# Performance work log

Hardware: AMD Instinct MI355X
Metric: run time of the kernel (lower is better)

The kernel has to match this reference:

```python
import jax, jax.numpy as jnp
import numpy as np

CLIP_LEN = 16
IN_CH = 64  # math.ceil(256 // 4 / 4) * 4
BN_EPS = 1e-5


def setup_inputs() -> dict:
    key = jax.random.key(0)
    ks = jax.random.split(key, 7)
    x = jax.random.normal(ks[0], (128, 256, 56, 56), jnp.float32)
    bn_gamma = 1.0 + 0.1 * jax.random.normal(ks[1], (IN_CH,), jnp.float32)
    bn_beta = 0.1 * jax.random.normal(ks[2], (IN_CH,), jnp.float32)
    bn_mean = 0.1 * jax.random.normal(ks[3], (IN_CH,), jnp.float32)
    bn_var = jax.random.uniform(ks[4], (IN_CH,), jnp.float32, minval=0.5, maxval=1.5)
    # groups=2 Conv3d: out=2, in_per_group=IN_CH//2, kernel 3x3x3
    conv_w = 0.02 * jax.random.normal(ks[5], (2, IN_CH // 2, 3, 3, 3), jnp.float32)
    conv_b = 0.02 * jax.random.normal(ks[6], (2,), jnp.float32)
    return dict(x=x, bn_gamma=bn_gamma, bn_beta=bn_beta, bn_mean=bn_mean,
                bn_var=bn_var, conv_w=conv_w, conv_b=conv_b)


def _gsm(x5, bn_gamma, bn_beta, bn_mean, bn_var, conv_w, conv_b):
    # x5: [n, c, t, h, w] with c == IN_CH
    n, c, t, h, w = x5.shape
    scale = bn_gamma * jax.lax.rsqrt(bn_var + BN_EPS)          # [c]
    shift = bn_beta - bn_mean * scale                          # [c]
    x_act = jax.nn.relu(x5 * scale[None, :, None, None, None]
                        + shift[None, :, None, None, None])
    gate = jnp.tanh(
        jax.lax.conv_general_dilated(
            x_act, conv_w, window_strides=(1, 1, 1), padding='SAME',
            dimension_numbers=('NCDHW', 'OIDHW', 'NCDHW'),
            feature_group_count=2)
        + conv_b[None, :, None, None, None])                   # [n,2,t,h,w]
    half = c // 2

    def gated_shift(xg, g, left):
        y = g * xg                                             # gated part
        r = xg - y                                             # residual part
        if left:
            y_sh = jnp.concatenate([y[:, :, 1:], jnp.zeros_like(y[:, :, :1])], axis=2)
        else:
            y_sh = jnp.concatenate([jnp.zeros_like(y[:, :, :1]), y[:, :, :-1]], axis=2)
        out = y_sh + r
        # channel regroup: [n,2,c/4,t,h,w] -> permute -> [n,c/2,t,h,w]
        return out.reshape(n, 2, half // 2, t, h, w).transpose(0, 2, 1, 3, 4, 5).reshape(n, half, t, h, w)

    y1 = gated_shift(x5[:, :half], gate[:, 0:1], left=True)
    y2 = gated_shift(x5[:, half:], gate[:, 1:2], left=False)
    return jnp.concatenate([y1, y2], axis=1)


def reference(x, bn_gamma, bn_beta, bn_mean, bn_var, conv_w, conv_b):
    nt, c, h, w = x.shape
    n = nt // CLIP_LEN
    # [nt, IN_CH, h, w] -> [n, IN_CH, T, h, w]
    xs = x[:, :IN_CH].reshape(n, CLIP_LEN, IN_CH, h, w).transpose(0, 2, 1, 3, 4)
    y = _gsm(xs, bn_gamma, bn_beta, bn_mean, bn_var, conv_w, conv_b)
    y = y.transpose(0, 2, 1, 3, 4).reshape(nt, IN_CH, h, w)
    # remaining channels pass through unchanged; net wrapper is identity
    return jnp.concatenate([y, x[:, IN_CH:]], axis=1)
```

## Files before the change

### kernel.cpp

```cpp
#include <hip/hip_runtime.h>
#include <math.h>

namespace {
constexpr int kT = 16;
constexpr int kH = 56;
constexpr int kW = 56;
constexpr int kCAll = 256;
constexpr int kPlane = kH * kW;
constexpr int kPlane4 = kPlane / 4;
constexpr size_t kGateBytes = (size_t)256 * kPlane * sizeof(float);
constexpr int kSpan = 192 * kPlane4;
constexpr int kFrame4 = kCAll * kPlane4;

typedef float nt4 __attribute__((ext_vector_type(4)));
}

__device__ __forceinline__ float4 nt_load4(const float4* p) {
  nt4 v = __builtin_nontemporal_load(reinterpret_cast<const nt4*>(p));
  return make_float4(v.x, v.y, v.z, v.w);
}
__device__ __forceinline__ void nt_store4(const float4& a, float4* p) {
  nt4 v = {a.x, a.y, a.z, a.w};
  __builtin_nontemporal_store(v, reinterpret_cast<nt4*>(p));
}


__device__ __forceinline__ void conv_block(
    int bid, int tid, const float* __restrict__ x,
    const float* __restrict__ gamma, const float* __restrict__ beta,
    const float* __restrict__ mean, const float* __restrict__ var,
    const float* __restrict__ cw, const float* __restrict__ cb,
    float* __restrict__ gate, float4* smb) {
  const int stripe = bid & 1;
  const int g = (bid >> 1) & 1;
  const int t = (bid >> 2) & 15;
  const int n = bid >> 6;
  const int h0 = stripe * 28;
  const int wid = tid >> 6;
  const int lane = tid & 63;
  const int r = lane >> 1;
  const int h = lane & 1;
  const int wbase = wid * 510;

  for (int i = lane; i < 510; i += 64)
    smb[wbase + i] = make_float4(0.f, 0.f, 0.f, 0.f);

  int rr_u[7], fb_u[7], go_u[7];
  bool val_u[7];
  #pragma unroll
  for (int u = 0; u < 7; ++u) {
    const int j = lane + u * 64;
    bool v = (j < 420);
    int rr = 0, fb = 0, go = 0;
    if (v) {
      rr = j / 14;
      fb = j - rr * 14;
      const int gr = h0 + rr - 1;
      v = ((unsigned)gr < (unsigned)kH);
      if (v) go = gr * 14 + fb;
    }
    rr_u[u] = rr; fb_u[u] = fb; go_u[u] = go; val_u[u] = v;
  }

  float acc[28];
  #pragma unroll
  for (int p = 0; p < 28; ++p) acc[p] = 0.f;

  auto loadS = [&](int s, float4 (&pf)[7]) {
    const int il = s / 3;
    const int kd = s - il * 3;
    const int tt = t + kd - 1;
    const int ch = g * 32 + wid * 8 + il;
    if (tt >= 0 && tt < kT) {
      const float4* src4 =
          (const float4*)x + ((size_t)(n * kT + tt) * kCAll + ch) * kPlane4;
      #pragma unroll
      for (int u = 0; u < 7; ++u)
        pf[u] = val_u[u] ? src4[go_u[u]] : make_float4(0.f, 0.f, 0.f, 0.f);
    } else {
      #pragma unroll
      for (int u = 0; u < 7; ++u) pf[u] = make_float4(0.f, 0.f, 0.f, 0.f);
    }
  };

  auto stageS = [&](int s, const float4 (&pf)[7]) {
    const int il = s / 3;
    const int kd = s - il * 3;
    const int tt = t + kd - 1;
    if (tt < 0 || tt >= kT) return;
    const int ch = g * 32 + wid * 8 + il;
    const float sc = gamma[ch] * rsqrtf(var[ch] + 1e-5f);
    const float sh = beta[ch] - mean[ch] * sc;
    #pragma unroll
    for (int u = 0; u < 7; ++u) {
      if (val_u[u]) {
        float4 a = pf[u];
        a.x = fmaxf(0.f, fmaf(a.x, sc, sh));
        a.y = fmaxf(0.f, fmaf(a.y, sc, sh));
        a.z = fmaxf(0.f, fmaf(a.z, sc, sh));
        a.w = fmaxf(0.f, fmaf(a.w, sc, sh));
        smb[wbase + rr_u[u] * 17 + fb_u[u] + 1] = a;
      }
    }
  };

  auto computeS = [&](int s) {
    const int il = s / 3;
    const int kd = s - il * 3;
    const int tt = t + kd - 1;
    if (tt < 0 || tt >= kT) return;
    if (r >= 28) return;
    const int ch = g * 32 + wid * 8 + il;
    const float* wbp = cw + ch * 27 + kd * 9;
    float wk[9];
    #pragma unroll
    for (int j = 0; j < 9; ++j) wk[j] = wbp[j];
    #pragma unroll
    for (int kh = 0; kh < 3; ++kh) {
      const int base = wbase + (r + kh) * 17 + 7 * h;
      float f[36];
      #pragma unroll
      for (int jj = 0; jj < 9; ++jj) {
        const float4 B = smb[base + jj];
        f[4 * jj + 0] = B.x; f[4 * jj + 1] = B.y;
        f[4 * jj + 2] = B.z; f[4 * jj + 3] = B.w;
      }
      const float w0 = wk[kh * 3 + 0];
      const float w1 = wk[kh * 3 + 1];
      const float w2 = wk[kh * 3 + 2];
      #pragma unroll
      for (int p = 0; p < 28; ++p)
        acc[p] = fmaf(f[p + 3], w0,
                 fmaf(f[p + 4], w1, fmaf(f[p + 5], w2, acc[p])));
    }
  };

  float4 A[7], B[7];
  loadS(0, A);
  for (int s2 = 0; s2 < 24; s2 += 2) {
    if (s2 + 1 < 24) loadS(s2 + 1, B);
    stageS(s2, A);
    computeS(s2);
    if (s2 + 2 < 24) loadS(s2 + 2, A);
    if (s2 + 1 < 24) { stageS(s2 + 1, B); computeS(s2 + 1); }
  }

  __syncthreads();
  float* smf = (float*)smb;
  if (r < 28) {
    const int q0 = r * 56 + h * 28;
    #pragma unroll
    for (int p = 0; p < 28; ++p) smf[wid * 1568 + q0 + p] = acc[p];
  }
  __syncthreads();
  const float bias = cb[g];
  float* gp = gate + ((size_t)(n * 2 + g) * kT + t) * kPlane + h0 * kW;
  for (int q = tid; q < 1568; q += 256) {
    float s = smf[q] + smf[1568 + q] + smf[2 * 1568 + q] + smf[3 * 1568 + q];
    gp[q] = tanhf(s + bias);
  }
}

__device__ __forceinline__ void copy_engine(
    int engine, int nengines, int tid, const float4* __restrict__ x4,
    float4* __restrict__ o4, int nf, int skip_hole) {
  const int wave = engine * 4 + (tid >> 6);
  const int lane = tid & 63;
  const int nwaves = nengines * 4;
  const size_t nsb = (size_t)nf * (kSpan / 512);
  for (size_t sb = wave; sb < nsb; sb += nwaves) {
    const size_t base = sb * 512 + lane;
    const int f = (int)(base / kSpan);
    const int within = (int)(base - (size_t)f * kSpan);
    const size_t gbase = (size_t)f * kFrame4 + 64 * kPlane4 + within;
    float4 v[8];
    #pragma unroll
    for (int u = 0; u < 8; ++u) v[u] = nt_load4(&x4[gbase + u * 64]);
    if (!skip_hole || f != 126) {
      #pragma unroll
      for (int u = 0; u < 8; ++u) nt_store4(v[u], &o4[gbase + u * 64]);
    } else {
      #pragma unroll
      for (int u = 0; u < 8; ++u)
        if (within + u * 64 >= 3 * kPlane4) nt_store4(v[u], &o4[gbase + u * 64]);
    }
  }
}

__global__ __launch_bounds__(256, 2)
void fused_conv_copy_kernel(const float* __restrict__ x,
                            const float* __restrict__ gamma,
                            const float* __restrict__ beta,
                            const float* __restrict__ mean,
                            const float* __restrict__ var,
                            const float* __restrict__ cw,
                            const float* __restrict__ cb,
                            float* __restrict__ gate,
                            const float4* __restrict__ x4,
                            float4* __restrict__ o4,
                            int nf_copy, int skip_hole) {
  __shared__ float4 smb[4 * 510];
  if ((blockIdx.x & 1) == 0) {
    copy_engine(blockIdx.x >> 1, 512, threadIdx.x, x4, o4, nf_copy, skip_hole);
    return;
  }
  conv_block(blockIdx.x >> 1, threadIdx.x, x, gamma, beta, mean, var, cw, cb,
             gate, smb);
}

__global__ __launch_bounds__(256)
void shift_columns_kernel(const float4* __restrict__ x4,
                          const float4* __restrict__ g4,
                          float4* __restrict__ o4) {
  const int q = blockIdx.x * 256 + threadIdx.x;
  const size_t xstep = (size_t)kFrame4;
  const int p = q % kPlane4;
  const int rem = q / kPlane4;
  const int m = rem & 31;
  const int half = (rem >> 5) & 1;
  const int n = rem >> 6;
  const int src_ch = half * 32 + m;
  const int k = 2 * (m & 15) + (m >> 4);
  const int c = half * 32 + k;
  const float4* xp = x4 + ((size_t)(n * kT) * kCAll + src_ch) * kPlane4 + p;
  const float4* gp = g4 + (size_t)((n * 2 + half) * kT) * kPlane4 + p;
  float4* op = o4 + ((size_t)(n * kT) * kCAll + c) * kPlane4 + p;
  if (half == 0) {
    float4 xc = nt_load4(&xp[0]);
    float4 gc = gp[0];
    #pragma unroll
    for (int t = 0; t < kT; ++t) {
      float4 xn = make_float4(0.f, 0.f, 0.f, 0.f);
      float4 gn = make_float4(0.f, 0.f, 0.f, 0.f);
      if (t < kT - 1) {
        xn = nt_load4(&xp[(size_t)(t + 1) * xstep]);
        gn = gp[(t + 1) * kPlane4];
      }
      float4 res;
      res.x = gn.x * xn.x + xc.x - gc.x * xc.x;
      res.y = gn.y * xn.y + xc.y - gc.y * xc.y;
      res.z = gn.z * xn.z + xc.z - gc.z * xc.z;
      res.w = gn.w * xn.w + xc.w - gc.w * xc.w;
      nt_store4(res, &op[(size_t)t * xstep]);
      xc = xn; gc = gn;
    }
  } else {
    float4 xprev = make_float4(0.f, 0.f, 0.f, 0.f);
    float4 gprev = make_float4(0.f, 0.f, 0.f, 0.f);
    #pragma unroll
    for (int t = 0; t < kT; ++t) {
      const float4 xc = nt_load4(&xp[(size_t)t * xstep]);
      const float4 gc = gp[t * kPlane4];
      float4 res;
      res.x = gprev.x * xprev.x + xc.x - gc.x * xc.x;
      res.y = gprev.y * xprev.y + xc.y - gc.y * xc.y;
      res.z = gprev.z * xprev.z + xc.z - gc.z * xc.z;
      res.w = gprev.w * xprev.w + xc.w - gc.w * xc.w;
      nt_store4(res, &op[(size_t)t * xstep]);
      xprev = xc; gprev = gc;
    }
  }
}

__global__ __launch_bounds__(256)
void copy_gate_slice_kernel(float4* __restrict__ o4) {
  const int j = blockIdx.x * 256 + threadIdx.x;
  if (j >= 3 * kPlane4) return;
  const int q = j / kPlane4;
  const int rr = j - q * kPlane4;
  const int pidx = (q == 0) ? 239 : (q == 1 ? 254 : 255);
  const size_t G1 = (size_t)127 * kCAll * kPlane4;
  const size_t H = ((size_t)126 * kCAll + 64) * kPlane4;
  o4[H + j] = o4[G1 + (size_t)pidx * kPlane4 + rr];
}

__global__ __launch_bounds__(256)
void shift_c64_kernel(const float4* __restrict__ x4,
                      const float4* __restrict__ g4,
                      float4* __restrict__ o4, int nf) {
  const size_t total = (size_t)nf * 64 * kPlane4;
  const size_t j = (size_t)blockIdx.x * 256 + threadIdx.x;
  if (j >= total) return;
  const int p = (int)(j % kPlane4);
  const size_t rest = j / kPlane4;
  const int c = (int)(rest % 64);
  const int f = (int)(rest / 64);
  const int n = f >> 4;
  const int t = f & 15;
  const int half = c >> 5;
  const int k = c & 31;
  const int m = ((k & 1) << 4) + (k >> 1);
  const int src_ch = half * 32 + m;
  const size_t xcur = ((size_t)f * kCAll + src_ch) * kPlane4 + p;
  const size_t gbase = (size_t)(n * 2 + half) * kT * kPlane4 + p;
  const float4 xc = x4[xcur];
  const float4 gc = g4[gbase + (size_t)t * kPlane4];
  float4 y = make_float4(0.f, 0.f, 0.f, 0.f);
  if (half == 0) {
    if (t < kT - 1) {
      const float4 xn = x4[xcur + (size_t)kCAll * kPlane4];
      const float4 gn = g4[gbase + (size_t)(t + 1) * kPlane4];
      y.x = gn.x * xn.x; y.y = gn.y * xn.y; y.z = gn.z * xn.z; y.w = gn.w * xn.w;
    }
  } else {
    if (t > 0) {
      const float4 xp = x4[xcur - (size_t)kCAll * kPlane4];
      const float4 gp = g4[gbase + (size_t)(t - 1) * kPlane4];
      y.x = gp.x * xp.x; y.y = gp.y * xp.y; y.z = gp.z * xp.z; y.w = gp.w * xp.w;
    }
  }
  const size_t oidx = ((size_t)f * kCAll + c) * kPlane4 + p;
  float4 res;
  res.x = y.x + (xc.x - gc.x * xc.x);
  res.y = y.y + (xc.y - gc.y * xc.y);
  res.z = y.z + (xc.z - gc.z * xc.z);
  res.w = y.w + (xc.w - gc.w * xc.w);
  o4[oidx] = res;
}

__global__ __launch_bounds__(256)
void last_frame_kernel(const float4* __restrict__ x4, float4* o4) {
  const int idx = blockIdx.x * 256 + threadIdx.x;
  if (idx >= kCAll * kPlane4) return;
  const size_t F127 = (size_t)127 * kCAll * kPlane4;
  const int p = idx % kPlane4;
  const int c = idx / kPlane4;
  if (c >= 64) { o4[F127 + idx] = x4[F127 + idx]; return; }
  const size_t H = ((size_t)126 * kCAll + 64) * kPlane4;
  const int half = c >> 5;
  const int k = c & 31;
  const int m = ((k & 1) << 4) + (k >> 1);
  const int src_ch = half * 32 + m;
  const float4 xc = x4[F127 + (size_t)src_ch * kPlane4 + p];
  float4 gc;
  float4 y = make_float4(0.f, 0.f, 0.f, 0.f);
  if (half == 0) {
    gc = o4[H + 0 * kPlane4 + p];
  } else {
    gc = o4[H + 2 * kPlane4 + p];
    const float4 gp = o4[H + 1 * kPlane4 + p];
    const float4 xp = x4[((size_t)126 * kCAll + src_ch) * kPlane4 + p];
    y.x = gp.x * xp.x; y.y = gp.y * xp.y; y.z = gp.z * xp.z; y.w = gp.w * xp.w;
  }
  float4 res;
  res.x = y.x + (xc.x - gc.x * xc.x);
  res.y = y.y + (xc.y - gc.y * xc.y);
  res.z = y.z + (xc.z - gc.z * xc.z);
  res.w = y.w + (xc.w - gc.w * xc.w);
  o4[F127 + idx] = res;
}

__global__ __launch_bounds__(256)
void fix_hole_kernel(const float4* __restrict__ x4, float4* __restrict__ o4) {
  const int j = blockIdx.x * 256 + threadIdx.x;
  if (j >= 3 * kPlane4) return;
  const size_t H = ((size_t)126 * kCAll + 64) * kPlane4;
  o4[H + j] = x4[H + j];
}

extern "C" void kernel_launch(void* const* d_in, const int* in_sizes, int n_in,
                              void* d_out, int out_size, void* d_ws, size_t ws_size,
                              hipStream_t stream) {
  const float* x     = (const float*)d_in[0];
  const float* gamma = (const float*)d_in[1];
  const float* beta  = (const float*)d_in[2];
  const float* mean  = (const float*)d_in[3];
  const float* var   = (const float*)d_in[4];
  const float* cw    = (const float*)d_in[5];
  const float* cb    = (const float*)d_in[6];
  float* out = (float*)d_out;
  const float4* x4v = (const float4*)x;
  float4* o4v = (float4*)out;

  const bool have_ws = (d_ws != nullptr) && (ws_size >= kGateBytes);
  float* gate = have_ws ? (float*)d_ws : out + (size_t)127 * kCAll * kPlane;
  const int nf = have_ws ? 128 : 127;
  const int skip_hole = have_ws ? 0 : 1;

  fused_conv_copy_kernel<<<1024, 256, 0, stream>>>(
      x, gamma, beta, mean, var, cw, cb, gate, x4v, o4v, nf, skip_hole);

  if (have_ws) {
    shift_columns_kernel<<<1568, 256, 0, stream>>>(
        x4v, (const float4*)gate, o4v);
  } else {
    copy_gate_slice_kernel<<<10, 256, 0, stream>>>(o4v);
    const int shift_total = nf * 64 * kPlane4;
    shift_c64_kernel<<<(shift_total + 255) / 256, 256, 0, stream>>>(
        x4v, (const float4*)gate, o4v, nf);
    last_frame_kernel<<<(kCAll * kPlane4 + 255) / 256, 256, 0, stream>>>(x4v, o4v);
    fix_hole_kernel<<<10, 256, 0, stream>>>(x4v, o4v);
  }
}
```

Measured before the change: 203.5 us.

## Replace static copy partition with atomic ticket-based dynamic work distribution

The pass-through copy of channels 64-255 is now distributed with a global atomic ticket counter instead of a static wave-strided assignment. Conv blocks join the copy work after they finish their gate computation, which is meant to balance load between conv and copy blocks. This adds a tiny counter-reset kernel launch and atomic traffic per group of four superblocks, and needs slightly more workspace.

Measured after the change: 279.3 us. 1.37x slower.

```diff
diff --git a/kernel.cpp b/kernel.cpp
--- a/kernel.cpp
+++ b/kernel.cpp
@@ -9,9 +9,10 @@
 constexpr int kPlane = kH * kW;
 constexpr int kPlane4 = kPlane / 4;
 constexpr size_t kGateBytes = (size_t)256 * kPlane * sizeof(float);
+constexpr size_t kWsNeed = kGateBytes + 256;
 constexpr int kSpan = 192 * kPlane4;
 constexpr int kFrame4 = kCAll * kPlane4;
-
+constexpr int kSbPerFrame = kSpan / 512;
 typedef float nt4 __attribute__((ext_vector_type(4)));
 }
 
@@ -161,13 +162,41 @@
   }
 }
 
-__device__ __forceinline__ void copy_engine(
+__device__ __forceinline__ void copy_superblock(
+    unsigned sb, int lane, const float4* __restrict__ x4,
+    float4* __restrict__ o4) {
+  const size_t base = (size_t)sb * 512 + lane;
+  const int f = (int)(base / kSpan);
+  const int within = (int)(base - (size_t)f * kSpan);
+  const size_t gbase = (size_t)f * kFrame4 + 64 * kPlane4 + within;
+  float4 v[8];
+  #pragma unroll
+  for (int u = 0; u < 8; ++u) v[u] = nt_load4(&x4[gbase + u * 64]);
+  #pragma unroll
+  for (int u = 0; u < 8; ++u) nt_store4(v[u], &o4[gbase + u * 64]);
+}
+
+__device__ __forceinline__ void copy_tickets(
+    int tid, unsigned* __restrict__ cnt, const float4* __restrict__ x4,
+    float4* __restrict__ o4, unsigned nsb) {
+  const int lane = tid & 63;
+  while (true) {
+    unsigned t0 = 0;
+    if (lane == 0) t0 = atomicAdd(cnt, 4u);
+    t0 = (unsigned)__shfl((int)t0, 0);
+    if (t0 >= nsb) break;
+    const unsigned end = min(nsb, t0 + 4u);
+    for (unsigned sb = t0; sb < end; ++sb) copy_superblock(sb, lane, x4, o4);
+  }
+}
+
+__device__ __forceinline__ void copy_engine_static(
     int engine, int nengines, int tid, const float4* __restrict__ x4,
     float4* __restrict__ o4, int nf, int skip_hole) {
   const int wave = engine * 4 + (tid >> 6);
   const int lane = tid & 63;
   const int nwaves = nengines * 4;
-  const size_t nsb = (size_t)nf * (kSpan / 512);
+  const size_t nsb = (size_t)nf * kSbPerFrame;
   for (size_t sb = wave; sb < nsb; sb += nwaves) {
     const size_t base = sb * 512 + lane;
     const int f = (int)(base / kSpan);
@@ -184,6 +213,33 @@
       for (int u = 0; u < 8; ++u)
         if (within + u * 64 >= 3 * kPlane4) nt_store4(v[u], &o4[gbase + u * 64]);
     }
+  }
+}
+
+__global__ void zero_counter_kernel(unsigned* __restrict__ cnt) {
+  if (threadIdx.x == 0) *cnt = 0u;
+}
+
+__global__ __launch_bounds__(256, 2)
+void fused_ws_kernel(const float* __restrict__ x,
+                     const float* __restrict__ gamma,
+                     const float* __restrict__ beta,
+                     const float* __restrict__ mean,
+                     const float* __restrict__ var,
+                     const float* __restrict__ cw,
+                     const float* __restrict__ cb,
+                     float* __restrict__ gate,
+                     const float4* __restrict__ x4,
+                     float4* __restrict__ o4,
+                     unsigned* __restrict__ cnt) {
+  __shared__ float4 smb[4 * 510];
+  const unsigned nsb = 128u * kSbPerFrame;
+  if (blockIdx.x & 1) {
+    conv_block(blockIdx.x >> 1, threadIdx.x, x, gamma, beta, mean, var, cw, cb,
+               gate, smb);
+    copy_tickets(threadIdx.x, cnt, x4, o4, nsb);
+  } else {
+    copy_tickets(threadIdx.x, cnt, x4, o4, nsb);
   }
 }
 
@@ -201,7 +257,8 @@
                             int nf_copy, int skip_hole) {
   __shared__ float4 smb[4 * 510];
   if ((blockIdx.x & 1) == 0) {
-    copy_engine(blockIdx.x >> 1, 512, threadIdx.x, x4, o4, nf_copy, skip_hole);
+    copy_engine_static(blockIdx.x >> 1, 512, threadIdx.x, x4, o4, nf_copy,
+                       skip_hole);
     return;
   }
   conv_block(blockIdx.x >> 1, threadIdx.x, x, gamma, beta, mean, var, cw, cb,
@@ -372,23 +429,26 @@
   const float4* x4v = (const float4*)x;
   float4* o4v = (float4*)out;
 
-  const bool have_ws = (d_ws != nullptr) && (ws_size >= kGateBytes);
-  float* gate = have_ws ? (float*)d_ws : out + (size_t)127 * kCAll * kPlane;
-  const int nf = have_ws ? 128 : 127;
-  const int skip_hole = have_ws ? 0 : 1;
-
-  fused_conv_copy_kernel<<<1024, 256, 0, stream>>>(
-      x, gamma, beta, mean, var, cw, cb, gate, x4v, o4v, nf, skip_hole);
+  const bool have_ws = (d_ws != nullptr) && (ws_size >= kWsNeed);
 
   if (have_ws) {
+    float* gate = (float*)d_ws;
+    unsigned* cnt = (unsigned*)((char*)d_ws + kGateBytes);
+    zero_counter_kernel<<<1, 64, 0, stream>>>(cnt);
+    fused_ws_kernel<<<1024, 256, 0, stream>>>(
+        x, gamma, beta, mean, var, cw, cb, gate, x4v, o4v, cnt);
     shift_columns_kernel<<<1568, 256, 0, stream>>>(
         x4v, (const float4*)gate, o4v);
-  } else {
-    copy_gate_slice_kernel<<<10, 256, 0, stream>>>(o4v);
-    const int shift_total = nf * 64 * kPlane4;
-    shift_c64_kernel<<<(shift_total + 255) / 256, 256, 0, stream>>>(
-        x4v, (const float4*)gate, o4v, nf);
-    last_frame_kernel<<<(kCAll * kPlane4 + 255) / 256, 256, 0, stream>>>(x4v, o4v);
-    fix_hole_kernel<<<10, 256, 0, stream>>>(x4v, o4v);
-  }
-}
+    return;
+  }
+
+  float* gate = out + (size_t)127 * kCAll * kPlane;
+  fused_conv_copy_kernel<<<1024, 256, 0, stream>>>(
+      x, gamma, beta, mean, var, cw, cb, gate, x4v, o4v, 127, 1);
+  copy_gate_slice_kernel<<<10, 256, 0, stream>>>(o4v);
+  const int shift_total = 127 * 64 * kPlane4;
+  shift_c64_kernel<<<(shift_total + 255) / 256, 256, 0, stream>>>(
+      x4v, (const float4*)gate, o4v, 127);
+  last_frame_kernel<<<(kCAll * kPlane4 + 255) / 256, 256, 0, stream>>>(x4v, o4v);
+  fix_hole_kernel<<<10, 256, 0, stream>>>(x4v, o4v);
+}
```
